# Kernel tuning notes

Measured on AMD Instinct MI355X. Metric: run time of the kernel, lower is better.

Reference implementation:

```python
import jax, jax.numpy as jnp
import numpy as np

EPS = 1e-8  # torch F.cosine_similarity eps


def setup_inputs() -> dict:
    key = jax.random.key(0)
    ks = jax.random.split(key, 10)
    S, B, V, D, H = 512, 128, 50257, 300, 512
    return {
        "context": jax.random.randint(ks[0], (32, B), 0, V),
        "ends": jax.random.randint(ks[1], (S, B), 0, V),
        "ends_ls": jax.random.randint(ks[2], (B,), 0, S),
        "embed_mat": jax.random.normal(ks[3], (V, D), jnp.float32),
        "w_ih": jax.random.normal(ks[4], (3 * H, 1), jnp.float32) * 0.05,
        "w_hh": jax.random.normal(ks[5], (3 * H, H), jnp.float32) * 0.05,
        "b_ih": jax.random.normal(ks[6], (3 * H,), jnp.float32) * 0.05,
        "b_hh": jax.random.normal(ks[7], (3 * H,), jnp.float32) * 0.05,
        "fc_w": jax.random.normal(ks[8], (1, H), jnp.float32) * 0.05,
        "fc_b": jax.random.normal(ks[9], (1,), jnp.float32) * 0.05,
    }


def _rep_features(embeds):
    # embeds: [S, B, D]. Causal max cosine similarity per position/batch.
    S = embeds.shape[0]
    norms = jnp.linalg.norm(embeds, axis=-1, keepdims=True)  # [S,B,1]
    xn = embeds / jnp.maximum(norms, EPS)
    sims = jnp.einsum("ibd,jbd->ijb", xn, xn)  # [S,S,B]
    sims = jnp.where(jnp.isnan(sims), -1.0, sims)  # sims[sims != sims] = -1
    i = jnp.arange(S)[:, None]
    j = jnp.arange(S)[None, :]
    causal = (j < i)[:, :, None]  # strictly past positions
    sims = jnp.where(causal, sims, -jnp.inf)
    feats = jnp.max(sims, axis=1)  # [S,B]
    feats = feats.at[0].set(0.0)  # position 0 -> zeros
    return feats


def _gru(x_seq, w_ih, w_hh, b_ih, b_hh, h0):
    # x_seq: [S, B, 1]; returns final hidden state [B, H]
    H = h0.shape[-1]

    def step(h, x):
        gi = x @ w_ih.T + b_ih  # [B, 3H]
        gh = h @ w_hh.T + b_hh
        ir, iz, inn = gi[:, :H], gi[:, H:2 * H], gi[:, 2 * H:]
        hr, hz, hn = gh[:, :H], gh[:, H:2 * H], gh[:, 2 * H:]
        r = jax.nn.sigmoid(ir + hr)
        z = jax.nn.sigmoid(iz + hz)
        n = jnp.tanh(inn + r * hn)
        h_new = (1.0 - z) * n + z * h
        return h_new, None

    h_last, _ = jax.lax.scan(step, h0, x_seq)
    return h_last


def reference(context, ends, ends_ls, embed_mat, w_ih, w_hh, b_ih, b_hh, fc_w, fc_b):
    S, B = ends.shape
    embeds = embed_mat[ends.reshape(-1)].reshape(S, B, -1)  # [S,B,D]
    feats = _rep_features(embeds)[:, :, None]  # [S,B,1]
    h0 = jnp.zeros((B, w_hh.shape[-1]), feats.dtype)
    h_last = _gru(feats, w_ih, w_hh, b_ih, b_hh, h0)  # [B,H]
    final = (h_last @ fc_w.T + fc_b).reshape(-1)  # [B]
    return final
```

## Files before the change

kernel.cpp:

```cpp
#include <hip/hip_runtime.h>
#include <hip/hip_bf16.h>
#include <math.h>

#define S_LEN 512
#define B_N   128
#define D_EMB 300
#define KP    320
#define H_N   512

typedef __attribute__((ext_vector_type(8)))  short short8;
typedef __attribute__((ext_vector_type(8)))  unsigned short ushort8;
typedef __attribute__((ext_vector_type(4)))  unsigned int uint4v;
typedef __attribute__((ext_vector_type(4)))  float float4v;
typedef __attribute__((ext_vector_type(16))) float float16v;

__device__ __forceinline__ unsigned short f32_to_bf16(float f) {
  unsigned u = __float_as_uint(f);
  u = (u + 0x7fffu + ((u >> 16) & 1u)) >> 16;
  return (unsigned short)u;
}
__device__ __forceinline__ float bf16_to_f32(unsigned short h) {
  return __uint_as_float(((unsigned)h) << 16);
}
__device__ __forceinline__ short8 as_short8(uint4v v) {
  union { uint4v u; short8 s; } c; c.u = v; return c.s;
}

__global__ __launch_bounds__(256) void k1_embed_norm(
    const int* __restrict__ ends, const float* __restrict__ emb,
    unsigned short* __restrict__ xh, unsigned short* __restrict__ xl) {
  int wave = threadIdx.x >> 6, lane = threadIdx.x & 63;
  int vec = blockIdx.x * 4 + wave;
  int b = vec & (B_N - 1), s = vec >> 7;
  int v = ends[vec];
  const float* row = emb + (size_t)v * D_EMB;
  float e0 = row[lane], e1 = row[lane + 64], e2 = row[lane + 128], e3 = row[lane + 192];
  float e4 = (lane + 256 < D_EMB) ? row[lane + 256] : 0.f;
  float ss = e0*e0 + e1*e1 + e2*e2 + e3*e3 + e4*e4;
  #pragma unroll
  for (int m = 1; m < 64; m <<= 1) ss += __shfl_xor(ss, m);
  float sc = 1.0f / fmaxf(sqrtf(ss), 1e-8f);
  size_t base = ((size_t)b * S_LEN + s) * KP;
  float xs[5] = { e0*sc, e1*sc, e2*sc, e3*sc, (lane + 256 < D_EMB) ? e4*sc : 0.f };
  #pragma unroll
  for (int i = 0; i < 5; ++i) {
    unsigned short hi = f32_to_bf16(xs[i]);
    unsigned short lo = f32_to_bf16(xs[i] - bf16_to_f32(hi));
    xh[base + lane + 64*i] = hi;
    xl[base + lane + 64*i] = lo;
  }
}

#define KC  80
#define LDP 88

__global__ __launch_bounds__(256) void k2_feats(
    const unsigned short* __restrict__ xh, const unsigned short* __restrict__ xl,
    float* __restrict__ feats) {
  __shared__ __align__(16) unsigned short sBh[64*LDP], sBl[64*LDP];
  __shared__ float rbuf[4][32];
  int b   = blockIdx.x;
  int ic  = blockIdx.y;
  int tid = threadIdx.x;
  int wave = tid >> 6, lane = tid & 63;
  int itl = wave & 1, jtl = wave >> 1;
  int itg = ic * 2 + itl;
  size_t xbase = (size_t)b * S_LEN * KP;
  int arow0 = ic * 64;
  const size_t arowoff = xbase + (size_t)(arow0 + itl * 32 + (lane & 31)) * KP
                       + (size_t)((lane >> 5) * 8);

  float rm[16];
  #pragma unroll
  for (int r = 0; r < 16; ++r) rm[r] = -INFINITY;

  for (int jc = 0; jc <= ic; ++jc) {
    int jt = jc * 2 + jtl;
    bool active = (jt <= itg);
    float16v acc;
    #pragma unroll
    for (int r = 0; r < 16; ++r) acc[r] = 0.f;

    for (int kc = 0; kc < 4; ++kc) {
      short8 a_h[5], a_l[5];
      #pragma unroll
      for (int ks = 0; ks < 5; ++ks) {
        size_t ga = arowoff + kc * KC + ks * 16;
        a_h[ks] = *(const short8*)&xh[ga];
        a_l[ks] = *(const short8*)&xl[ga];
      }
      __syncthreads();
      for (int u = tid; u < 640; u += 256) {
        int r = u / 10, sg = u % 10;
        size_t gb = xbase + (size_t)(jc*64 + r) * KP + kc*KC + sg*8;
        int la = r * LDP + sg * 8;
        *(ushort8*)&sBh[la] = *(const ushort8*)&xh[gb];
        *(ushort8*)&sBl[la] = *(const ushort8*)&xl[gb];
      }
      __syncthreads();
      if (active) {
        int br = (jtl*32 + (lane & 31)) * LDP;
        int kq = (lane >> 5) * 8;
        #pragma unroll
        for (int ks = 0; ks < 5; ++ks) {
          short8 b_h = *(const short8*)&sBh[br + ks*16 + kq];
          short8 b_l = *(const short8*)&sBl[br + ks*16 + kq];
          acc = __builtin_amdgcn_mfma_f32_32x32x16_bf16(a_h[ks], b_h, acc, 0, 0, 0);
          acc = __builtin_amdgcn_mfma_f32_32x32x16_bf16(a_h[ks], b_l, acc, 0, 0, 0);
          acc = __builtin_amdgcn_mfma_f32_32x32x16_bf16(a_l[ks], b_h, acc, 0, 0, 0);
        }
      }
    }
    if (active) {
      int colg = jt * 32 + (lane & 31);
      #pragma unroll
      for (int r = 0; r < 16; ++r) {
        int rowg = itg * 32 + (r & 3) + 8*(r >> 2) + 4*(lane >> 5);
        float v = acc[r];
        if (jt == itg && colg >= rowg) v = -INFINITY;
        rm[r] = fmaxf(rm[r], v);
      }
    }
  }
  #pragma unroll
  for (int r = 0; r < 16; ++r) {
    float v = rm[r];
    v = fmaxf(v, __shfl_xor(v, 1));
    v = fmaxf(v, __shfl_xor(v, 2));
    v = fmaxf(v, __shfl_xor(v, 4));
    v = fmaxf(v, __shfl_xor(v, 8));
    v = fmaxf(v, __shfl_xor(v, 16));
    rm[r] = v;
  }
  if ((lane & 31) == 0) {
    int half = lane >> 5;
    #pragma unroll
    for (int r = 0; r < 16; ++r)
      rbuf[wave][(r & 3) + 8*(r >> 2) + 4*half] = rm[r];
  }
  __syncthreads();
  if (tid < 64) {
    int it2 = tid >> 5, rl = tid & 31;
    float v = fmaxf(rbuf[it2][rl], rbuf[it2 + 2][rl]);
    int i = ic * 64 + it2 * 32 + rl;
    feats[i * B_N + b] = (i == 0) ? 0.0f : v;
  }
}

#define HW64 (B_N * H_N / 2)

__global__ __launch_bounds__(512, 1) void k3_gru(
    const float* __restrict__ feats,
    const float* __restrict__ w_ih, const float* __restrict__ w_hh,
    const float* __restrict__ b_ih, const float* __restrict__ b_hh,
    const float* __restrict__ fc_w, const float* __restrict__ fc_b,
    unsigned long long* __restrict__ hq, unsigned int* __restrict__ bars,
    float* __restrict__ out) {
  __shared__ __align__(16) float4v red2[8][16][16];
  __shared__ float osum[256];
  int tid = threadIdx.x;
  int wave = tid >> 6, lane = tid & 63;
  int g = blockIdx.x & 7, s = blockIdx.x >> 3;

  short8 wfh[3][2], wfl[3][2];
  {
    int nloc = lane & 15;
    int kq = (lane >> 4) * 8;
    #pragma unroll
    for (int gt = 0; gt < 3; ++gt) {
      const float* wr = w_hh + (size_t)(gt * H_N + s * 16 + nloc) * H_N;
      #pragma unroll
      for (int ks = 0; ks < 2; ++ks) {
        int k0 = wave * 64 + ks * 32 + kq;
        short8 h8, l8;
        #pragma unroll
        for (int j = 0; j < 8; ++j) {
          float wv = wr[k0 + j];
          unsigned short hi = f32_to_bf16(wv);
          unsigned short lo = f32_to_bf16(wv - bf16_to_f32(hi));
          h8[j] = (short)hi; l8[j] = (short)lo;
        }
        wfh[gt][ks] = h8; wfl[gt][ks] = l8;
      }
    }
  }
  const bool gater = (tid < 256);
  int bb = tid >> 4, jj = tid & 15;
  int jr = s * 16 + jj;
  float wihr = w_ih[jr], wihz = w_ih[H_N + jr], wihn = w_ih[2*H_N + jr];
  float bir = b_ih[jr],  biz = b_ih[H_N + jr],  bin_ = b_ih[2*H_N + jr];
  float bhr = b_hh[jr],  bhz = b_hh[H_N + jr],  bhn = b_hh[2*H_N + jr];
  float fcw = fc_w[jr];
  int gb = g * 16 + (bb & 15);
  float h_old = 0.f;
  const unsigned int* fp = bars + g * 32 + wave * 4 + (lane & 3);
  unsigned int* myflag = bars + g * 32 + s;

  const int Cp = g * 16 + (s >> 3) * 4 + ((s >> 1) & 3);
  const int qp = (2 * s + (jj >> 3)) & 3;
  const size_t prodoff = (size_t)Cp * 512 + (size_t)qp * 128 + (size_t)(bb & 15) * 8;
  const size_t cbase = (size_t)(g * 16 + wave * 2) * 512 + (size_t)lane * 8;

  for (int t = 0; t < S_LEN; ++t) {
    float x = gater ? feats[t * B_N + gb] : 0.f;
    float sr = 0.f, sz = 0.f, sn = 0.f;
    if (t > 0) {
      {
        const unsigned tgt = (unsigned)t;
        for (;;) {
          unsigned f = __hip_atomic_load(fp, __ATOMIC_RELAXED, __HIP_MEMORY_SCOPE_AGENT);
          if (__ballot(f < tgt) == 0ull) break;
          __builtin_amdgcn_s_sleep(1);
        }
        asm volatile("" ::: "memory");
      }
      const unsigned short* hh =
          (const unsigned short*)(hq + (size_t)((t - 1) & 1) * HW64);
      const unsigned short* hbase = hh + cbase;
      const unsigned short* lbase = hbase + 65536;
      uint4v rh0, rh1, rl0, rl1;
      asm volatile(
        "global_load_dwordx4 %0, %4, off sc1\n\t"
        "global_load_dwordx4 %1, %4, off offset:1024 sc1\n\t"
        "global_load_dwordx4 %2, %5, off sc1\n\t"
        "global_load_dwordx4 %3, %5, off offset:1024 sc1\n\t"
        "s_waitcnt vmcnt(0)"
        : "=&v"(rh0), "=&v"(rh1), "=&v"(rl0), "=&v"(rl1)
        : "v"(hbase), "v"(lbase)
        : "memory");
      short8 ah0 = as_short8(rh0), ah1 = as_short8(rh1);
      short8 al0 = as_short8(rl0), al1 = as_short8(rl1);
      float4v a0, a1, a2;
      #pragma unroll
      for (int r = 0; r < 4; ++r) { a0[r] = 0.f; a1[r] = 0.f; a2[r] = 0.f; }
      a0 = __builtin_amdgcn_mfma_f32_16x16x32_bf16(ah0, wfh[0][0], a0, 0,0,0);
      a1 = __builtin_amdgcn_mfma_f32_16x16x32_bf16(ah0, wfh[1][0], a1, 0,0,0);
      a2 = __builtin_amdgcn_mfma_f32_16x16x32_bf16(ah0, wfh[2][0], a2, 0,0,0);
      a0 = __builtin_amdgcn_mfma_f32_16x16x32_bf16(ah0, wfl[0][0], a0, 0,0,0);
      a1 = __builtin_amdgcn_mfma_f32_16x16x32_bf16(ah0, wfl[1][0], a1, 0,0,0);
      a2 = __builtin_amdgcn_mfma_f32_16x16x32_bf16(ah0, wfl[2][0], a2, 0,0,0);
      a0 = __builtin_amdgcn_mfma_f32_16x16x32_bf16(al0, wfh[0][0], a0, 0,0,0);
      a1 = __builtin_amdgcn_mfma_f32_16x16x32_bf16(al0, wfh[1][0], a1, 0,0,0);
      a2 = __builtin_amdgcn_mfma_f32_16x16x32_bf16(al0, wfh[2][0], a2, 0,0,0);
      a0 = __builtin_amdgcn_mfma_f32_16x16x32_bf16(ah1, wfh[0][1], a0, 0,0,0);
      a1 = __builtin_amdgcn_mfma_f32_16x16x32_bf16(ah1, wfh[1][1], a1, 0,0,0);
      a2 = __builtin_amdgcn_mfma_f32_16x16x32_bf16(ah1, wfh[2][1], a2, 0,0,0);
      a0 = __builtin_amdgcn_mfma_f32_16x16x32_bf16(ah1, wfl[0][1], a0, 0,0,0);
      a1 = __builtin_amdgcn_mfma_f32_16x16x32_bf16(ah1, wfl[1][1], a1, 0,0,0);
      a2 = __builtin_amdgcn_mfma_f32_16x16x32_bf16(ah1, wfl[2][1], a2, 0,0,0);
      a0 = __builtin_amdgcn_mfma_f32_16x16x32_bf16(al1, wfh[0][1], a0, 0,0,0);
      a1 = __builtin_amdgcn_mfma_f32_16x16x32_bf16(al1, wfh[1][1], a1, 0,0,0);
      a2 = __builtin_amdgcn_mfma_f32_16x16x32_bf16(al1, wfh[2][1], a2, 0,0,0);
      int colw = lane & 15, roww = (lane >> 4) * 4;
      #pragma unroll
      for (int r = 0; r < 4; ++r) {
        float4v w; w[0] = a0[r]; w[1] = a1[r]; w[2] = a2[r]; w[3] = 0.f;
        red2[wave][roww + r][colw] = w;
      }
      __syncthreads();
      if (gater) {
        float4v sv = red2[0][bb][jj];
        #pragma unroll
        for (int w8 = 1; w8 < 8; ++w8) sv += red2[w8][bb][jj];
        sr = sv[0]; sz = sv[1]; sn = sv[2];
      }
    }
    if (gater) {
      float ar_ = fminf(fmaxf(x * wihr + bir + sr + bhr, -30.f), 30.f);
      float az_ = fminf(fmaxf(x * wihz + biz + sz + bhz, -30.f), 30.f);
      float r_ = __builtin_amdgcn_rcpf(1.f + __expf(-ar_));
      float z_ = __builtin_amdgcn_rcpf(1.f + __expf(-az_));
      float an_ = fminf(fmaxf(x * wihn + bin_ + r_ * (sn + bhn), -30.f), 30.f);
      float en = __expf(-2.f * an_);
      float n_ = (1.f - en) * __builtin_amdgcn_rcpf(1.f + en);
      float h_new = (1.f - z_) * n_ + z_ * h_old;
      h_old = h_new;
      if (t < S_LEN - 1) {
        unsigned short hi16 = f32_to_bf16(h_new);
        unsigned short lo16 = f32_to_bf16(h_new - bf16_to_f32(hi16));
        unsigned myh = hi16, myl = lo16;
        unsigned oh = (unsigned)__shfl_xor((int)myh, 1);
        unsigned ol = (unsigned)__shfl_xor((int)myl, 1);
        bool od1 = (jj & 1) != 0;
        unsigned pH = od1 ? (oh | (myh << 16)) : (myh | (oh << 16));
        unsigned pL = od1 ? (ol | (myl << 16)) : (myl | (ol << 16));
        unsigned qh = (unsigned)__shfl_xor((int)pH, 2);
        unsigned ql = (unsigned)__shfl_xor((int)pL, 2);
        bool od2 = (jj & 2) != 0;
        unsigned h01 = od2 ? qh : pH, h23 = od2 ? pH : qh;
        unsigned l01 = od2 ? ql : pL, l23 = od2 ? pL : ql;
        unsigned xh01 = (unsigned)__shfl_xor((int)h01, 4);
        unsigned xh23 = (unsigned)__shfl_xor((int)h23, 4);
        unsigned xl01 = (unsigned)__shfl_xor((int)l01, 4);
        unsigned xl23 = (unsigned)__shfl_xor((int)l23, 4);
        bool od4 = (jj & 4) != 0;
        uint4v runH, runL;
        runH[0] = od4 ? xh01 : h01; runH[1] = od4 ? xh23 : h23;
        runH[2] = od4 ? h01 : xh01; runH[3] = od4 ? h23 : xh23;
        runL[0] = od4 ? xl01 : l01; runL[1] = od4 ? xl23 : l23;
        runL[2] = od4 ? l01 : xl01; runL[3] = od4 ? l23 : xl23;
        unsigned short* hh = (unsigned short*)(hq + (size_t)(t & 1) * HW64);
        if ((jj & 3) == 0) {
          if ((jj & 4) == 0) *(uint4v*)(hh + prodoff)         = runH;
          else               *(uint4v*)(hh + 65536 + prodoff) = runL;
        }
      }
    }
    if (t < S_LEN - 1) {
      asm volatile("s_waitcnt vmcnt(0)" ::: "memory");
      __syncthreads();
      if (tid == 0)
        __hip_atomic_store(myflag, (unsigned)(t + 1),
                           __ATOMIC_RELAXED, __HIP_MEMORY_SCOPE_WORKGROUP);
    }
  }
  if (gater) osum[tid] = h_old * fcw;
  __syncthreads();
  if (gater && jj == 0) {
    float acc = 0.f;
    #pragma unroll
    for (int q = 0; q < 16; ++q) acc += osum[bb * 16 + q];
    if (s == 0) acc += fc_b[0];
    atomicAdd(&out[gb], acc);
  }
}

extern "C" void kernel_launch(void* const* d_in, const int* in_sizes, int n_in,
                              void* d_out, int out_size, void* d_ws, size_t ws_size,
                              hipStream_t stream) {
  (void)in_sizes; (void)n_in; (void)out_size; (void)ws_size;
  const int*   ends = (const int*)d_in[1];
  const float* emb  = (const float*)d_in[3];
  const float* w_ih = (const float*)d_in[4];
  const float* w_hh = (const float*)d_in[5];
  const float* b_ih = (const float*)d_in[6];
  const float* b_hh = (const float*)d_in[7];
  const float* fc_w = (const float*)d_in[8];
  const float* fc_b = (const float*)d_in[9];
  float* out = (float*)d_out;

  size_t xn_elems = (size_t)B_N * S_LEN * KP;
  unsigned short* xh = (unsigned short*)d_ws;
  unsigned short* xl = xh + xn_elems;
  float* feats = (float*)(xl + xn_elems);
  unsigned long long* hq = (unsigned long long*)(feats + S_LEN * B_N);
  unsigned int* bars = (unsigned int*)(hq + 2 * (size_t)HW64);

  hipMemsetAsync(out, 0, sizeof(float) * B_N, stream);
  hipMemsetAsync(bars, 0, 4096, stream);

  k1_embed_norm<<<dim3(S_LEN * B_N / 4), dim3(256), 0, stream>>>(ends, emb, xh, xl);
  k2_feats<<<dim3(B_N, 8), dim3(256), 0, stream>>>(xh, xl, feats);

  void* args[] = { (void*)&feats, (void*)&w_ih, (void*)&w_hh, (void*)&b_ih,
                   (void*)&b_hh, (void*)&fc_w, (void*)&fc_b,
                   (void*)&hq, (void*)&bars, (void*)&out };
  hipLaunchCooperativeKernel((void*)k3_gru, dim3(256), dim3(512), args, 0, stream);
}
```

Measured before the change: 1.093 ms.

## Halve GRU grid so each block owns 32 hidden units per batch group

The persistent cooperative GRU kernel now runs 128 blocks instead of 256. Each block handles 32 hidden units, using two 16-column MFMA tiles per gate, and all 512 threads now compute gates where only half did before. The per-group flag barrier waits on 16 producers instead of 32, and the packed hidden-state layout is simplified to match the new slicing. This aims to cut cross-block synchronisation cost and idle threads per timestep. In exchange, each block does twice the MFMA work per step, which lengthens the serial compute on the critical path.

```diff
diff --git a/kernel.cpp b/kernel.cpp
--- a/kernel.cpp
+++ b/kernel.cpp
@@ -156,53 +156,54 @@
     const float* __restrict__ fc_w, const float* __restrict__ fc_b,
     unsigned long long* __restrict__ hq, unsigned int* __restrict__ bars,
     float* __restrict__ out) {
-  __shared__ __align__(16) float4v red2[8][16][16];
-  __shared__ float osum[256];
+  __shared__ __align__(16) float4v red2[16][16][16];
+  __shared__ float osum[512];
   int tid = threadIdx.x;
   int wave = tid >> 6, lane = tid & 63;
   int g = blockIdx.x & 7, s = blockIdx.x >> 3;
 
-  short8 wfh[3][2], wfl[3][2];
+  short8 wfh[3][2][2], wfl[3][2][2];
   {
     int nloc = lane & 15;
     int kq = (lane >> 4) * 8;
     #pragma unroll
     for (int gt = 0; gt < 3; ++gt) {
-      const float* wr = w_hh + (size_t)(gt * H_N + s * 16 + nloc) * H_N;
-      #pragma unroll
-      for (int ks = 0; ks < 2; ++ks) {
-        int k0 = wave * 64 + ks * 32 + kq;
-        short8 h8, l8;
+      #pragma unroll
+      for (int nt = 0; nt < 2; ++nt) {
+        const float* wr = w_hh + (size_t)(gt * H_N + s * 32 + nt * 16 + nloc) * H_N;
         #pragma unroll
-        for (int j = 0; j < 8; ++j) {
-          float wv = wr[k0 + j];
-          unsigned short hi = f32_to_bf16(wv);
-          unsigned short lo = f32_to_bf16(wv - bf16_to_f32(hi));
-          h8[j] = (short)hi; l8[j] = (short)lo;
+        for (int ks = 0; ks < 2; ++ks) {
+          int k0 = wave * 64 + ks * 32 + kq;
+          short8 h8, l8;
+          #pragma unroll
+          for (int j = 0; j < 8; ++j) {
+            float wv = wr[k0 + j];
+            unsigned short hi = f32_to_bf16(wv);
+            unsigned short lo = f32_to_bf16(wv - bf16_to_f32(hi));
+            h8[j] = (short)hi; l8[j] = (short)lo;
+          }
+          wfh[gt][ks][nt] = h8; wfl[gt][ks][nt] = l8;
         }
-        wfh[gt][ks] = h8; wfl[gt][ks] = l8;
-      }
-    }
-  }
-  const bool gater = (tid < 256);
-  int bb = tid >> 4, jj = tid & 15;
-  int jr = s * 16 + jj;
+      }
+    }
+  }
+  int bb = tid >> 5, jj = tid & 31;
+  int jr = s * 32 + jj;
   float wihr = w_ih[jr], wihz = w_ih[H_N + jr], wihn = w_ih[2*H_N + jr];
   float bir = b_ih[jr],  biz = b_ih[H_N + jr],  bin_ = b_ih[2*H_N + jr];
   float bhr = b_hh[jr],  bhz = b_hh[H_N + jr],  bhn = b_hh[2*H_N + jr];
   float fcw = fc_w[jr];
-  int gb = g * 16 + (bb & 15);
+  int gb = g * 16 + bb;
   float h_old = 0.f;
-  const unsigned int* fp = bars + g * 32 + wave * 4 + (lane & 3);
-  unsigned int* myflag = bars + g * 32 + s;
-
-  const int Cp = g * 16 + (s >> 3) * 4 + ((s >> 1) & 3);
-  const int qp = (2 * s + (jj >> 3)) & 3;
-  const size_t prodoff = (size_t)Cp * 512 + (size_t)qp * 128 + (size_t)(bb & 15) * 8;
+  const unsigned int* fp = bars + g * 16 + wave * 2 + (lane & 1);
+  unsigned int* myflag = bars + g * 16 + s;
+
+  const size_t prodoff = (size_t)(g * 16 + s) * 512
+                       + (size_t)(jj >> 3) * 128 + (size_t)bb * 8;
   const size_t cbase = (size_t)(g * 16 + wave * 2) * 512 + (size_t)lane * 8;
 
   for (int t = 0; t < S_LEN; ++t) {
-    float x = gater ? feats[t * B_N + gb] : 0.f;
+    float x = feats[t * B_N + gb];
     float sr = 0.f, sz = 0.f, sn = 0.f;
     if (t > 0) {
       {
@@ -230,83 +231,100 @@
         : "memory");
       short8 ah0 = as_short8(rh0), ah1 = as_short8(rh1);
       short8 al0 = as_short8(rl0), al1 = as_short8(rl1);
-      float4v a0, a1, a2;
-      #pragma unroll
-      for (int r = 0; r < 4; ++r) { a0[r] = 0.f; a1[r] = 0.f; a2[r] = 0.f; }
-      a0 = __builtin_amdgcn_mfma_f32_16x16x32_bf16(ah0, wfh[0][0], a0, 0,0,0);
-      a1 = __builtin_amdgcn_mfma_f32_16x16x32_bf16(ah0, wfh[1][0], a1, 0,0,0);
-      a2 = __builtin_amdgcn_mfma_f32_16x16x32_bf16(ah0, wfh[2][0], a2, 0,0,0);
-      a0 = __builtin_amdgcn_mfma_f32_16x16x32_bf16(ah0, wfl[0][0], a0, 0,0,0);
-      a1 = __builtin_amdgcn_mfma_f32_16x16x32_bf16(ah0, wfl[1][0], a1, 0,0,0);
-      a2 = __builtin_amdgcn_mfma_f32_16x16x32_bf16(ah0, wfl[2][0], a2, 0,0,0);
-      a0 = __builtin_amdgcn_mfma_f32_16x16x32_bf16(al0, wfh[0][0], a0, 0,0,0);
-      a1 = __builtin_amdgcn_mfma_f32_16x16x32_bf16(al0, wfh[1][0], a1, 0,0,0);
-      a2 = __builtin_amdgcn_mfma_f32_16x16x32_bf16(al0, wfh[2][0], a2, 0,0,0);
-      a0 = __builtin_amdgcn_mfma_f32_16x16x32_bf16(ah1, wfh[0][1], a0, 0,0,0);
-      a1 = __builtin_amdgcn_mfma_f32_16x16x32_bf16(ah1, wfh[1][1], a1, 0,0,0);
-      a2 = __builtin_amdgcn_mfma_f32_16x16x32_bf16(ah1, wfh[2][1], a2, 0,0,0);
-      a0 = __builtin_amdgcn_mfma_f32_16x16x32_bf16(ah1, wfl[0][1], a0, 0,0,0);
-      a1 = __builtin_amdgcn_mfma_f32_16x16x32_bf16(ah1, wfl[1][1], a1, 0,0,0);
-      a2 = __builtin_amdgcn_mfma_f32_16x16x32_bf16(ah1, wfl[2][1], a2, 0,0,0);
-      a0 = __builtin_amdgcn_mfma_f32_16x16x32_bf16(al1, wfh[0][1], a0, 0,0,0);
-      a1 = __builtin_amdgcn_mfma_f32_16x16x32_bf16(al1, wfh[1][1], a1, 0,0,0);
-      a2 = __builtin_amdgcn_mfma_f32_16x16x32_bf16(al1, wfh[2][1], a2, 0,0,0);
+      float4v a00, a01, a02, a10, a11, a12;
+      #pragma unroll
+      for (int r = 0; r < 4; ++r) {
+        a00[r]=0.f; a01[r]=0.f; a02[r]=0.f; a10[r]=0.f; a11[r]=0.f; a12[r]=0.f;
+      }
+      a00 = __builtin_amdgcn_mfma_f32_16x16x32_bf16(ah0, wfh[0][0][0], a00, 0,0,0);
+      a01 = __builtin_amdgcn_mfma_f32_16x16x32_bf16(ah0, wfh[1][0][0], a01, 0,0,0);
+      a02 = __builtin_amdgcn_mfma_f32_16x16x32_bf16(ah0, wfh[2][0][0], a02, 0,0,0);
+      a10 = __builtin_amdgcn_mfma_f32_16x16x32_bf16(ah0, wfh[0][0][1], a10, 0,0,0);
+      a11 = __builtin_amdgcn_mfma_f32_16x16x32_bf16(ah0, wfh[1][0][1], a11, 0,0,0);
+      a12 = __builtin_amdgcn_mfma_f32_16x16x32_bf16(ah0, wfh[2][0][1], a12, 0,0,0);
+      a00 = __builtin_amdgcn_mfma_f32_16x16x32_bf16(ah0, wfl[0][0][0], a00, 0,0,0);
+      a01 = __builtin_amdgcn_mfma_f32_16x16x32_bf16(ah0, wfl[1][0][0], a01, 0,0,0);
+      a02 = __builtin_amdgcn_mfma_f32_16x16x32_bf16(ah0, wfl[2][0][0], a02, 0,0,0);
+      a10 = __builtin_amdgcn_mfma_f32_16x16x32_bf16(ah0, wfl[0][0][1], a10, 0,0,0);
+      a11 = __builtin_amdgcn_mfma_f32_16x16x32_bf16(ah0, wfl[1][0][1], a11, 0,0,0);
+      a12 = __builtin_amdgcn_mfma_f32_16x16x32_bf16(ah0, wfl[2][0][1], a12, 0,0,0);
+      a00 = __builtin_amdgcn_mfma_f32_16x16x32_bf16(al0, wfh[0][0][0], a00, 0,0,0);
+      a01 = __builtin_amdgcn_mfma_f32_16x16x32_bf16(al0, wfh[1][0][0], a01, 0,0,0);
+      a02 = __builtin_amdgcn_mfma_f32_16x16x32_bf16(al0, wfh[2][0][0], a02, 0,0,0);
+      a10 = __builtin_amdgcn_mfma_f32_16x16x32_bf16(al0, wfh[0][0][1], a10, 0,0,0);
+      a11 = __builtin_amdgcn_mfma_f32_16x16x32_bf16(al0, wfh[1][0][1], a11, 0,0,0);
+      a12 = __builtin_amdgcn_mfma_f32_16x16x32_bf16(al0, wfh[2][0][1], a12, 0,0,0);
+      a00 = __builtin_amdgcn_mfma_f32_16x16x32_bf16(ah1, wfh[0][1][0], a00, 0,0,0);
+      a01 = __builtin_amdgcn_mfma_f32_16x16x32_bf16(ah1, wfh[1][1][0], a01, 0,0,0);
+      a02 = __builtin_amdgcn_mfma_f32_16x16x32_bf16(ah1, wfh[2][1][0], a02, 0,0,0);
+      a10 = __builtin_amdgcn_mfma_f32_16x16x32_bf16(ah1, wfh[0][1][1], a10, 0,0,0);
+      a11 = __builtin_amdgcn_mfma_f32_16x16x32_bf16(ah1, wfh[1][1][1], a11, 0,0,0);
+      a12 = __builtin_amdgcn_mfma_f32_16x16x32_bf16(ah1, wfh[2][1][1], a12, 0,0,0);
+      a00 = __builtin_amdgcn_mfma_f32_16x16x32_bf16(ah1, wfl[0][1][0], a00, 0,0,0);
+      a01 = __builtin_amdgcn_mfma_f32_16x16x32_bf16(ah1, wfl[1][1][0], a01, 0,0,0);
+      a02 = __builtin_amdgcn_mfma_f32_16x16x32_bf16(ah1, wfl[2][1][0], a02, 0,0,0);
+      a10 = __builtin_amdgcn_mfma_f32_16x16x32_bf16(ah1, wfl[0][1][1], a10, 0,0,0);
+      a11 = __builtin_amdgcn_mfma_f32_16x16x32_bf16(ah1, wfl[1][1][1], a11, 0,0,0);
+      a12 = __builtin_amdgcn_mfma_f32_16x16x32_bf16(ah1, wfl[2][1][1], a12, 0,0,0);
+      a00 = __builtin_amdgcn_mfma_f32_16x16x32_bf16(al1, wfh[0][1][0], a00, 0,0,0);
+      a01 = __builtin_amdgcn_mfma_f32_16x16x32_bf16(al1, wfh[1][1][0], a01, 0,0,0);
+      a02 = __builtin_amdgcn_mfma_f32_16x16x32_bf16(al1, wfh[2][1][0], a02, 0,0,0);
+      a10 = __builtin_amdgcn_mfma_f32_16x16x32_bf16(al1, wfh[0][1][1], a10, 0,0,0);
+      a11 = __builtin_amdgcn_mfma_f32_16x16x32_bf16(al1, wfh[1][1][1], a11, 0,0,0);
+      a12 = __builtin_amdgcn_mfma_f32_16x16x32_bf16(al1, wfh[2][1][1], a12, 0,0,0);
       int colw = lane & 15, roww = (lane >> 4) * 4;
       #pragma unroll
       for (int r = 0; r < 4; ++r) {
-        float4v w; w[0] = a0[r]; w[1] = a1[r]; w[2] = a2[r]; w[3] = 0.f;
-        red2[wave][roww + r][colw] = w;
+        float4v w0; w0[0] = a00[r]; w0[1] = a01[r]; w0[2] = a02[r]; w0[3] = 0.f;
+        float4v w1; w1[0] = a10[r]; w1[1] = a11[r]; w1[2] = a12[r]; w1[3] = 0.f;
+        red2[wave * 2 + 0][roww + r][colw] = w0;
+        red2[wave * 2 + 1][roww + r][colw] = w1;
       }
       __syncthreads();
-      if (gater) {
-        float4v sv = red2[0][bb][jj];
-        #pragma unroll
-        for (int w8 = 1; w8 < 8; ++w8) sv += red2[w8][bb][jj];
-        sr = sv[0]; sz = sv[1]; sn = sv[2];
-      }
-    }
-    if (gater) {
-      float ar_ = fminf(fmaxf(x * wihr + bir + sr + bhr, -30.f), 30.f);
-      float az_ = fminf(fmaxf(x * wihz + biz + sz + bhz, -30.f), 30.f);
-      float r_ = __builtin_amdgcn_rcpf(1.f + __expf(-ar_));
-      float z_ = __builtin_amdgcn_rcpf(1.f + __expf(-az_));
-      float an_ = fminf(fmaxf(x * wihn + bin_ + r_ * (sn + bhn), -30.f), 30.f);
-      float en = __expf(-2.f * an_);
-      float n_ = (1.f - en) * __builtin_amdgcn_rcpf(1.f + en);
-      float h_new = (1.f - z_) * n_ + z_ * h_old;
-      h_old = h_new;
-      if (t < S_LEN - 1) {
-        unsigned short hi16 = f32_to_bf16(h_new);
-        unsigned short lo16 = f32_to_bf16(h_new - bf16_to_f32(hi16));
-        unsigned myh = hi16, myl = lo16;
-        unsigned oh = (unsigned)__shfl_xor((int)myh, 1);
-        unsigned ol = (unsigned)__shfl_xor((int)myl, 1);
-        bool od1 = (jj & 1) != 0;
-        unsigned pH = od1 ? (oh | (myh << 16)) : (myh | (oh << 16));
-        unsigned pL = od1 ? (ol | (myl << 16)) : (myl | (ol << 16));
-        unsigned qh = (unsigned)__shfl_xor((int)pH, 2);
-        unsigned ql = (unsigned)__shfl_xor((int)pL, 2);
-        bool od2 = (jj & 2) != 0;
-        unsigned h01 = od2 ? qh : pH, h23 = od2 ? pH : qh;
-        unsigned l01 = od2 ? ql : pL, l23 = od2 ? pL : ql;
-        unsigned xh01 = (unsigned)__shfl_xor((int)h01, 4);
-        unsigned xh23 = (unsigned)__shfl_xor((int)h23, 4);
-        unsigned xl01 = (unsigned)__shfl_xor((int)l01, 4);
-        unsigned xl23 = (unsigned)__shfl_xor((int)l23, 4);
-        bool od4 = (jj & 4) != 0;
-        uint4v runH, runL;
-        runH[0] = od4 ? xh01 : h01; runH[1] = od4 ? xh23 : h23;
-        runH[2] = od4 ? h01 : xh01; runH[3] = od4 ? h23 : xh23;
-        runL[0] = od4 ? xl01 : l01; runL[1] = od4 ? xl23 : l23;
-        runL[2] = od4 ? l01 : xl01; runL[3] = od4 ? l23 : xl23;
-        unsigned short* hh = (unsigned short*)(hq + (size_t)(t & 1) * HW64);
-        if ((jj & 3) == 0) {
-          if ((jj & 4) == 0) *(uint4v*)(hh + prodoff)         = runH;
-          else               *(uint4v*)(hh + 65536 + prodoff) = runL;
-        }
-      }
-    }
+      int ntc = jj >> 4, colc = jj & 15;
+      float4v sv = red2[ntc][bb][colc];
+      #pragma unroll
+      for (int w8 = 1; w8 < 8; ++w8) sv += red2[w8 * 2 + ntc][bb][colc];
+      sr = sv[0]; sz = sv[1]; sn = sv[2];
+    }
+    float ar_ = fminf(fmaxf(x * wihr + bir + sr + bhr, -30.f), 30.f);
+    float az_ = fminf(fmaxf(x * wihz + biz + sz + bhz, -30.f), 30.f);
+    float r_ = __builtin_amdgcn_rcpf(1.f + __expf(-ar_));
+    float z_ = __builtin_amdgcn_rcpf(1.f + __expf(-az_));
+    float an_ = fminf(fmaxf(x * wihn + bin_ + r_ * (sn + bhn), -30.f), 30.f);
+    float en = __expf(-2.f * an_);
+    float n_ = (1.f - en) * __builtin_amdgcn_rcpf(1.f + en);
+    float h_new = (1.f - z_) * n_ + z_ * h_old;
+    h_old = h_new;
     if (t < S_LEN - 1) {
+      unsigned short hi16 = f32_to_bf16(h_new);
+      unsigned short lo16 = f32_to_bf16(h_new - bf16_to_f32(hi16));
+      unsigned myh = hi16, myl = lo16;
+      unsigned oh = (unsigned)__shfl_xor((int)myh, 1);
+      unsigned ol = (unsigned)__shfl_xor((int)myl, 1);
+      bool od1 = (jj & 1) != 0;
+      unsigned pH = od1 ? (oh | (myh << 16)) : (myh | (oh << 16));
+      unsigned pL = od1 ? (ol | (myl << 16)) : (myl | (ol << 16));
+      unsigned qh = (unsigned)__shfl_xor((int)pH, 2);
+      unsigned ql = (unsigned)__shfl_xor((int)pL, 2);
+      bool od2 = (jj & 2) != 0;
+      unsigned h01 = od2 ? qh : pH, h23 = od2 ? pH : qh;
+      unsigned l01 = od2 ? ql : pL, l23 = od2 ? pL : ql;
+      unsigned xh01 = (unsigned)__shfl_xor((int)h01, 4);
+      unsigned xh23 = (unsigned)__shfl_xor((int)h23, 4);
+      unsigned xl01 = (unsigned)__shfl_xor((int)l01, 4);
+      unsigned xl23 = (unsigned)__shfl_xor((int)l23, 4);
+      bool od4 = (jj & 4) != 0;
+      uint4v runH, runL;
+      runH[0] = od4 ? xh01 : h01; runH[1] = od4 ? xh23 : h23;
+      runH[2] = od4 ? h01 : xh01; runH[3] = od4 ? h23 : xh23;
+      runL[0] = od4 ? xl01 : l01; runL[1] = od4 ? xl23 : l23;
+      runL[2] = od4 ? l01 : xl01; runL[3] = od4 ? l23 : xl23;
+      unsigned short* hh = (unsigned short*)(hq + (size_t)(t & 1) * HW64);
+      if ((jj & 3) == 0) {
+        if ((jj & 4) == 0) *(uint4v*)(hh + prodoff)         = runH;
+        else               *(uint4v*)(hh + 65536 + prodoff) = runL;
+      }
       asm volatile("s_waitcnt vmcnt(0)" ::: "memory");
       __syncthreads();
       if (tid == 0)
@@ -314,12 +332,12 @@
                            __ATOMIC_RELAXED, __HIP_MEMORY_SCOPE_WORKGROUP);
     }
   }
-  if (gater) osum[tid] = h_old * fcw;
+  osum[tid] = h_old * fcw;
   __syncthreads();
-  if (gater && jj == 0) {
+  if (jj == 0) {
     float acc = 0.f;
     #pragma unroll
-    for (int q = 0; q < 16; ++q) acc += osum[bb * 16 + q];
+    for (int q = 0; q < 32; ++q) acc += osum[bb * 32 + q];
     if (s == 0) acc += fc_b[0];
     atomicAdd(&out[gb], acc);
   }
@@ -355,5 +373,5 @@
   void* args[] = { (void*)&feats, (void*)&w_ih, (void*)&w_hh, (void*)&b_ih,
                    (void*)&b_hh, (void*)&fc_w, (void*)&fc_b,
                    (void*)&hq, (void*)&bars, (void*)&out };
-  hipLaunchCooperativeKernel((void*)k3_gru, dim3(256), dim3(512), args, 0, stream);
-}
+  hipLaunchCooperativeKernel((void*)k3_gru, dim3(128), dim3(512), args, 0, stream);
+}
```

Measured after the change: 1.313 ms. 1.2x slower.

## Double-buffer LDS tiles in k2_feats and launch heaviest row chunks first

Applied to the files above, without the earlier changes.

The k2_feats loop over j-chunks and k-chunks is flattened into one loop with two LDS buffers. The next B tile is loaded from global memory while MFMAs run on the current one, which cuts the two barriers per step down to one. The block-to-row-chunk mapping is also reversed so the blocks with the most causal work start first, easing load imbalance in the triangular workload. LDS use doubles, which could lower occupancy.

```diff
diff --git a/kernel.cpp b/kernel.cpp
--- a/kernel.cpp
+++ b/kernel.cpp
@@ -57,10 +57,10 @@
 __global__ __launch_bounds__(256) void k2_feats(
     const unsigned short* __restrict__ xh, const unsigned short* __restrict__ xl,
     float* __restrict__ feats) {
-  __shared__ __align__(16) unsigned short sBh[64*LDP], sBl[64*LDP];
+  __shared__ __align__(16) unsigned short sBh[2][64*LDP], sBl[2][64*LDP];
   __shared__ float rbuf[4][32];
   int b   = blockIdx.x;
-  int ic  = blockIdx.y;
+  int ic  = 7 - blockIdx.y;
   int tid = threadIdx.x;
   int wave = tid >> 6, lane = tid & 63;
   int itl = wave & 1, jtl = wave >> 1;
@@ -74,14 +74,37 @@
   #pragma unroll
   for (int r = 0; r < 16; ++r) rm[r] = -INFINITY;
 
-  for (int jc = 0; jc <= ic; ++jc) {
+  const int NT = (ic + 1) * 4;
+
+  for (int u = tid; u < 640; u += 256) {
+    int r = u / 10, sg = u % 10;
+    size_t gb = xbase + (size_t)r * KP + sg * 8;
+    int la = r * LDP + sg * 8;
+    *(ushort8*)&sBh[0][la] = *(const ushort8*)&xh[gb];
+    *(ushort8*)&sBl[0][la] = *(const ushort8*)&xl[gb];
+  }
+  __syncthreads();
+
+  float16v acc;
+  for (int n = 0; n < NT; ++n) {
+    int jc = n >> 2, kc = n & 3, buf = n & 1;
+    if (kc == 0) {
+      #pragma unroll
+      for (int r = 0; r < 16; ++r) acc[r] = 0.f;
+    }
+    if (n + 1 < NT) {
+      int jn = (n + 1) >> 2, kn = (n + 1) & 3;
+      for (int u = tid; u < 640; u += 256) {
+        int r = u / 10, sg = u % 10;
+        size_t gb = xbase + (size_t)(jn * 64 + r) * KP + kn * KC + sg * 8;
+        int la = r * LDP + sg * 8;
+        *(ushort8*)&sBh[buf ^ 1][la] = *(const ushort8*)&xh[gb];
+        *(ushort8*)&sBl[buf ^ 1][la] = *(const ushort8*)&xl[gb];
+      }
+    }
     int jt = jc * 2 + jtl;
     bool active = (jt <= itg);
-    float16v acc;
-    #pragma unroll
-    for (int r = 0; r < 16; ++r) acc[r] = 0.f;
-
-    for (int kc = 0; kc < 4; ++kc) {
+    if (active) {
       short8 a_h[5], a_l[5];
       #pragma unroll
       for (int ks = 0; ks < 5; ++ks) {
@@ -89,29 +112,19 @@
         a_h[ks] = *(const short8*)&xh[ga];
         a_l[ks] = *(const short8*)&xl[ga];
       }
-      __syncthreads();
-      for (int u = tid; u < 640; u += 256) {
-        int r = u / 10, sg = u % 10;
-        size_t gb = xbase + (size_t)(jc*64 + r) * KP + kc*KC + sg*8;
-        int la = r * LDP + sg * 8;
-        *(ushort8*)&sBh[la] = *(const ushort8*)&xh[gb];
-        *(ushort8*)&sBl[la] = *(const ushort8*)&xl[gb];
-      }
-      __syncthreads();
-      if (active) {
-        int br = (jtl*32 + (lane & 31)) * LDP;
-        int kq = (lane >> 5) * 8;
-        #pragma unroll
-        for (int ks = 0; ks < 5; ++ks) {
-          short8 b_h = *(const short8*)&sBh[br + ks*16 + kq];
-          short8 b_l = *(const short8*)&sBl[br + ks*16 + kq];
-          acc = __builtin_amdgcn_mfma_f32_32x32x16_bf16(a_h[ks], b_h, acc, 0, 0, 0);
-          acc = __builtin_amdgcn_mfma_f32_32x32x16_bf16(a_h[ks], b_l, acc, 0, 0, 0);
-          acc = __builtin_amdgcn_mfma_f32_32x32x16_bf16(a_l[ks], b_h, acc, 0, 0, 0);
-        }
-      }
-    }
-    if (active) {
+      int br = (jtl * 32 + (lane & 31)) * LDP;
+      int kq = (lane >> 5) * 8;
+      #pragma unroll
+      for (int ks = 0; ks < 5; ++ks) {
+        short8 b_h = *(const short8*)&sBh[buf][br + ks*16 + kq];
+        short8 b_l = *(const short8*)&sBl[buf][br + ks*16 + kq];
+        acc = __builtin_amdgcn_mfma_f32_32x32x16_bf16(a_h[ks], b_h, acc, 0, 0, 0);
+        acc = __builtin_amdgcn_mfma_f32_32x32x16_bf16(a_h[ks], b_l, acc, 0, 0, 0);
+        acc = __builtin_amdgcn_mfma_f32_32x32x16_bf16(a_l[ks], b_h, acc, 0, 0, 0);
+      }
+    }
+    __syncthreads();
+    if (kc == 3 && active) {
       int colg = jt * 32 + (lane & 31);
       #pragma unroll
       for (int r = 0; r < 16; ++r) {
```

New measurement: 1.070 ms. 1.02x faster.
